# Kernel optimization log

Hardware: AMD Instinct MI355X
Metric: run time of the kernel (lower is better)

Reference implementation:

```python
import jax, jax.numpy as jnp
import numpy as np

# Model constants (from Equilibrium3BConfig + hardcoded MambaBlock args)
D_MODEL = 2560
D_INNER = 5120          # expand=2
N_STATE = 128           # d_state
HEADS = 80              # d_inner // headdim
P_HEAD = 64             # headdim
D_CONV = 4
CONV_DIM = D_INNER + 2 * N_STATE        # 5376 (x, B, C share the conv)
D_IN_PROJ = 2 * D_INNER + 2 * N_STATE + HEADS  # 10576 (z, xBC, dt)
N_EXPERTS = 16
TOP_K = 2
M_INTER = 864
MS_INTER = 1728
EPS = 1e-6


def _rms(x, w, eps=EPS):
    xf = x.astype(jnp.float32)
    xf = xf * jax.lax.rsqrt(jnp.mean(xf * xf, axis=-1, keepdims=True) + eps)
    return w * xf.astype(x.dtype)


def setup_inputs() -> dict:
    key = jax.random.key(0)
    ks = jax.random.split(key, 16)
    b, l = 1, 1024
    s = 0.02  # weight scale, keeps activations sane through the deep block
    return {
        "hidden_states": jax.random.normal(ks[0], (b, l, D_MODEL), jnp.float32),
        "w_in": jax.random.normal(ks[1], (D_MODEL, D_IN_PROJ), jnp.float32) * s,
        "conv_w": jax.random.normal(ks[2], (CONV_DIM, D_CONV), jnp.float32) * s,
        "conv_b": jnp.zeros((CONV_DIM,), jnp.float32),
        "dt_bias": jax.random.normal(ks[3], (HEADS,), jnp.float32) * s,
        "A_log": jax.random.normal(ks[4], (HEADS,), jnp.float32) * s,
        "D": jnp.ones((HEADS,), jnp.float32),
        "mamba_norm_w": jnp.ones((D_INNER,), jnp.float32),
        "w_out": jax.random.normal(ks[5], (D_INNER, D_MODEL), jnp.float32) * s,
        "ln1_w": jnp.ones((D_MODEL,), jnp.float32),
        "ln2_w": jnp.ones((D_MODEL,), jnp.float32),
        "router_w": jax.random.normal(ks[6], (D_MODEL, N_EXPERTS), jnp.float32) * s,
        "we_gate": jax.random.normal(ks[7], (N_EXPERTS, D_MODEL, M_INTER), jnp.float32) * s,
        "we_up": jax.random.normal(ks[8], (N_EXPERTS, D_MODEL, M_INTER), jnp.float32) * s,
        "we_down": jax.random.normal(ks[9], (N_EXPERTS, M_INTER, D_MODEL), jnp.float32) * s,
        "ws_gate": jax.random.normal(ks[10], (D_MODEL, MS_INTER), jnp.float32) * s,
        "ws_up": jax.random.normal(ks[11], (D_MODEL, MS_INTER), jnp.float32) * s,
        "ws_down": jax.random.normal(ks[12], (MS_INTER, D_MODEL), jnp.float32) * s,
    }


def _forward(hidden_states, w_in, conv_w, conv_b, dt_bias, A_log, D, mamba_norm_w,
             w_out, ln1_w, ln2_w, router_w, we_gate, we_up, we_down,
             ws_gate, ws_up, ws_down):
    b, l, d = hidden_states.shape

    # ---- Mamba2 (selective scan) sub-block ----
    residual = hidden_states
    x = _rms(hidden_states, ln1_w)
    zxbcdt = x @ w_in  # [b, l, 10576]
    z, xBC, dt = jnp.split(zxbcdt, [D_INNER, D_INNER + CONV_DIM], axis=-1)

    # depthwise causal conv over (x, B, C) channels, then SiLU
    xBC_t = xBC.transpose(0, 2, 1)  # [b, c, l]
    conv = jax.lax.conv_general_dilated(
        xBC_t, conv_w[:, None, :], (1,), [(D_CONV - 1, 0)],
        feature_group_count=CONV_DIM, dimension_numbers=("NCH", "OIH", "NCH"))
    xBC = jax.nn.silu((conv + conv_b[None, :, None]).transpose(0, 2, 1))
    xs, Bc, Cc = jnp.split(xBC, [D_INNER, D_INNER + N_STATE], axis=-1)

    dt = jax.nn.softplus(dt + dt_bias)          # [b, l, h]
    A = -jnp.exp(A_log)                          # [h]
    xh = xs.reshape(b, l, HEADS, P_HEAD)

    # time-major for scan
    dt_l = dt.transpose(1, 0, 2)                 # [l, b, h]
    xh_l = xh.transpose(1, 0, 2, 3)              # [l, b, h, p]
    B_l = Bc.transpose(1, 0, 2)                  # [l, b, n]
    C_l = Cc.transpose(1, 0, 2)                  # [l, b, n]

    def step(h, inp):
        dt_t, x_t, B_t, C_t = inp
        dA = jnp.exp(dt_t * A)                   # [b, h]
        h = h * dA[..., None, None] + (dt_t[..., None] * x_t)[..., None] * B_t[:, None, None, :]
        y = jnp.einsum("bhpn,bn->bhp", h, C_t)
        return h, y

    h0 = jnp.zeros((b, HEADS, P_HEAD, N_STATE), hidden_states.dtype)
    _, y_l = jax.lax.scan(step, h0, (dt_l, xh_l, B_l, C_l))
    y_l = y_l + D[None, None, :, None] * xh_l    # skip term
    y = y_l.transpose(1, 0, 2, 3).reshape(b, l, D_INNER)
    y = _rms(y * jax.nn.silu(z), mamba_norm_w)   # gated RMSNorm
    hidden = residual + y @ w_out

    # ---- DeepSeekMoE sub-block ----
    residual2 = hidden
    xm = _rms(hidden, ln2_w).reshape(b * l, d)
    logits = xm @ router_w
    probs = jax.nn.softmax(logits.astype(jnp.float32), axis=-1)
    topv, topi = jax.lax.top_k(probs, TOP_K)
    topv = topv / jnp.sum(topv, axis=-1, keepdims=True)  # renormalize top-k
    wdense = jnp.sum(jax.nn.one_hot(topi, N_EXPERTS, dtype=xm.dtype)
                     * topv[..., None].astype(xm.dtype), axis=1)  # [T, E]

    # routed experts (SwiGLU), dense-masked faithful math
    hexp = (jax.nn.silu(jnp.einsum("td,edm->tem", xm, we_gate))
            * jnp.einsum("td,edm->tem", xm, we_up))
    y_routed = jnp.einsum("tem,emd,te->td", hexp, we_down, wdense)

    # shared experts (single fused SwiGLU MLP)
    y_shared = (jax.nn.silu(xm @ ws_gate) * (xm @ ws_up)) @ ws_down

    moe = (y_routed + y_shared).reshape(b, l, d)
    return residual2 + moe


def reference(hidden_states, w_in, conv_w, conv_b, dt_bias, A_log, D, mamba_norm_w,
              w_out, ln1_w, ln2_w, router_w, we_gate, we_up, we_down,
              ws_gate, ws_up, ws_down):
    return _forward(hidden_states, w_in, conv_w, conv_b, dt_bias, A_log, D,
                    mamba_norm_w, w_out, ln1_w, ln2_w, router_w,
                    we_gate, we_up, we_down, ws_gate, ws_up, ws_down)
```

## Files before the change

### kernel.cpp

```cpp
#include <hip/hip_runtime.h>

typedef __attribute__((ext_vector_type(4))) float f32x4;
typedef __attribute__((ext_vector_type(8))) __bf16 bf16x8;
typedef __attribute__((ext_vector_type(4))) __bf16 bf16x4;
typedef __attribute__((ext_vector_type(8))) _Float16 f16x8;
typedef __attribute__((ext_vector_type(4))) _Float16 f16x4;

#define D_MODEL 2560
#define D_INNER 5120
#define N_STATE 128
#define HEADS 80
#define P_HEAD 64
#define CONV_DIM 5376
#define D_INPROJ 10576
#define SEQ 1024
#define NCHUNK 16
#define QCHUNK 64
#define NEXP 16
#define M_INTER 864
#define MS_INTER 1728
#define NSLOT 2048
#define NSLOTP 2176

__device__ __forceinline__ float siluf(float x) { return x / (1.f + __expf(-x)); }

__device__ __forceinline__ int swz_p(int k4, int P) {
  return (k4 & ~31) | ((((k4 >> 3) & 3) ^ P) << 3) | (k4 & 7);
}
__device__ __forceinline__ int swz64(int k4, int row) {
  return (k4 & ~63) | (((((k4 >> 3) & 7) ^ (row & 7)) << 3)) | (k4 & 7);
}

__device__ __forceinline__ void gl16(const __bf16* g, __bf16* l) {
  __builtin_amdgcn_global_load_lds((const __attribute__((address_space(1))) unsigned int*)g,
                                   (__attribute__((address_space(3))) unsigned int*)l, 16, 0, 0);
}

__device__ __forceinline__ float block_sum256(float v, float* red) {
#pragma unroll
  for (int m = 32; m > 0; m >>= 1) v += __shfl_xor(v, m, 64);
  int w = threadIdx.x >> 6;
  if ((threadIdx.x & 63) == 0) red[w] = v;
  __syncthreads();
  return red[0] + red[1] + red[2] + red[3];
}

template <bool FP16>
__global__ __launch_bounds__(256) void k_rmsnorm_p(const float* __restrict__ in,
                                                   const float* __restrict__ w,
                                                   float* __restrict__ f32out,
                                                   __bf16* __restrict__ ph,
                                                   __bf16* __restrict__ pdh,
                                                   __bf16* __restrict__ pdl, int D) {
  __shared__ float red[4];
  int t = blockIdx.x, tid = threadIdx.x;
  const float* x = in + (size_t)t * D;
  int nd4 = D >> 2;
  float ss = 0.f;
  for (int i = tid; i < nd4; i += 256) {
    float4 v = ((const float4*)x)[i];
    ss += v.x * v.x + v.y * v.y + v.z * v.z + v.w * v.w;
  }
  float tot = block_sum256(ss, red);
  float r = rsqrtf(tot / (float)D + 1e-6f);
  int P = (t >> 1) & 3;
  for (int i = tid; i < nd4; i += 256) {
    float4 v = ((const float4*)x)[i];
    float4 wv = ((const float4*)w)[i];
    float4 o;
    o.x = wv.x * v.x * r; o.y = wv.y * v.y * r; o.z = wv.z * v.z * r; o.w = wv.w * v.w * r;
// ... 25 lines not shown
                                                __bf16* __restrict__ Th, __bf16* __restrict__ Tl) {
  __shared__ float T[64][65];
  const int n0 = blockIdx.x * 64, k0 = blockIdx.y * 64, tid = threadIdx.x;
#pragma unroll
  for (int i = 0; i < 16; i++) {
    int idx = tid + i * 256;
    int k = idx >> 6, n = idx & 63;
    float v = 0.f;
    if (n0 + n < N) v = W[(size_t)(k0 + k) * ld + n0 + n];
    T[k][n] = v;
  }
  __syncthreads();
#pragma unroll
  for (int i = 0; i < 4; i++) {
    int idx = tid + i * 256;
    int n = idx >> 4, p4 = (idx & 15) * 4;
    int nn = n0 + n;
    if constexpr (SPLIT) {
      int P = (nn >> 1) & 3;
      bf16x4 hv, lv;
#pragma unroll
      for (int e = 0; e < 4; e++) {
        int p = p4 + e;
        int kk = (p & ~31) | ((((p >> 3) & 3) ^ P) << 3) | (p & 7);
        float v = T[kk][n];
        __bf16 h = (__bf16)v;
        hv[e] = h;
        lv[e] = (__bf16)(v - (float)h);
      }
      *(bf16x4*)&Th[(size_t)nn * K + k0 + p4] = hv;
      *(bf16x4*)&Tl[(size_t)nn * K + k0 + p4] = lv;
    } else if constexpr (FP16) {
      f16x4 hv;
#pragma unroll
      for (int e = 0; e < 4; e++) {
        int p = p4 + e;
        int kk = swz64(p, nn);
        hv[e] = (_Float16)T[kk][n];
      }
      *(f16x4*)&Th[(size_t)nn * K + k0 + p4] = hv;
    } else {
      bf16x4 hv;
#pragma unroll
      for (int e = 0; e < 4; e++) {
        int p = p4 + e;
        int kk = swz64(p, nn);
        hv[e] = (__bf16)T[kk][n];
      }
      *(bf16x4*)&Th[(size_t)nn * K + k0 + p4] = hv;
    }
  }
}

template <bool SPLIT, bool FP16, int BK>
__global__ __launch_bounds__(256) void k_gemm2(const __bf16* __restrict__ Ah,
                                               const __bf16* __restrict__ Al,
                                               const __bf16* __restrict__ Bh,
                                               const __bf16* __restrict__ Bl,
                                               float* __restrict__ C,
                                               int M, int N, int K, int ks, int nst) {
  constexpr int PLE = 128 * BK;
  constexpr int NPL = SPLIT ? 4 : 2;
  constexpr int CALLS = PLE / 2048;
  constexpr int CPR = BK / 8;
  constexpr int RPC = 256 / CPR;
  constexpr int KSUB = BK / 32;
  __shared__ __bf16 lds[NPL * PLE];
  __bf16* const AsH = lds;
  __bf16* const BsH = lds + (SPLIT ? 2 : 1) * PLE;
  __bf16* const AsL = SPLIT ? (lds + PLE) : nullptr;
  __bf16* const BsL = SPLIT ? (lds + 3 * PLE) : nullptr;

  const int tid = threadIdx.x;
  const int T = gridDim.x * gridDim.y * gridDim.z;
  const int linear = blockIdx.x + gridDim.x * (blockIdx.y + gridDim.y * blockIdx.z);
  const int s_idx = (linear & 7) * (T >> 3) + (linear >> 3);
  const int bm = s_idx & 7;
  const int g = s_idx >> 3;
  const int bn = g % gridDim.y;
  const int z = g / gridDim.y;

  const int m0 = bm * 128, n0 = bn * 128;
  const int s0 = (int)(((long long)z * nst) / ks);
  const int s1 = (int)(((long long)(z + 1) * nst) / ks);
  float* __restrict__ Cp = C + (size_t)z * M * N;

  const int lane = tid & 63, wid = tid >> 6;
  const int wr = wid >> 1, wc = wid & 1;
  const int l16 = lane & 15, kl = lane >> 4;

  const int srow = tid / CPR;
  const int schunk = (tid % CPR) * 8;
  size_t aB[CALLS], bB[CALLS];
#pragma unroll
  for (int i = 0; i < CALLS; i++) {
    aB[i] = (size_t)(m0 + srow + RPC * i) * K + schunk;
    bB[i] = (size_t)(n0 + srow + RPC * i) * K + schunk;
  }

  int aoff[4][KSUB], boff[4][KSUB];
#pragma unroll
  for (int mi = 0; mi < 4; mi++) {
    int ra = wr * 64 + mi * 16 + l16;
    int rb = wc * 64 + mi * 16 + l16;
#pragma unroll
    for (int kk = 0; kk < KSUB; kk++) {
      if constexpr (BK == 32) {
        aoff[mi][kk] = ra * 64 + ((kl ^ ((ra >> 1) & 3)) << 4);
        boff[mi][kk] = rb * 64 + ((kl ^ ((rb >> 1) & 3)) << 4);
      } else {
        aoff[mi][kk] = ra * (2 * BK) + (((kk * 4 + kl) ^ (ra & 7)) << 4);
        boff[mi][kk] = rb * (2 * BK) + (((kk * 4 + kl) ^ (rb & 7)) << 4);
      }
    }
  }

  f32x4 acc[4][4];
#pragma unroll
  for (int mi = 0; mi < 4; mi++)
#pragma unroll
    for (int ni = 0; ni < 4; ni++) acc[mi][ni] = f32x4{0.f, 0.f, 0.f, 0.f};

  for (int s = s0; s < s1; ++s) {
    const int kof = s * BK;
    __syncthreads();
#pragma unroll
    for (int i = 0; i < CALLS; i++) {
      gl16(Ah + aB[i] + kof, AsH + (tid + i * 256) * 8);
      gl16(Bh + bB[i] + kof, BsH + (tid + i * 256) * 8);
      if constexpr (SPLIT) {
        gl16(Al + aB[i] + kof, AsL + (tid + i * 256) * 8);
        gl16(Bl + bB[i] + kof, BsL + (tid + i * 256) * 8);
      }
    }
    __syncthreads();
#pragma unroll
    for (int kk = 0; kk < KSUB; kk++) {
      if constexpr (!SPLIT && FP16) {
        f16x8 ah[4], bh[4];
#pragma unroll
        for (int mi = 0; mi < 4; mi++) ah[mi] = *(const f16x8*)((const char*)AsH + aoff[mi][kk]);
#pragma unroll
        for (int ni = 0; ni < 4; ni++) bh[ni] = *(const f16x8*)((const char*)BsH + boff[ni][kk]);
#pragma unroll
        for (int mi = 0; mi < 4; mi++)
#pragma unroll
          for (int ni = 0; ni < 4; ni++)
            acc[mi][ni] = __builtin_amdgcn_mfma_f32_16x16x32_f16(ah[mi], bh[ni], acc[mi][ni], 0, 0, 0);
      } else {
        bf16x8 ah[4], bh[4];
#pragma unroll
        for (int mi = 0; mi < 4; mi++) ah[mi] = *(const bf16x8*)((const char*)AsH + aoff[mi][kk]);
#pragma unroll
        for (int ni = 0; ni < 4; ni++) bh[ni] = *(const bf16x8*)((const char*)BsH + boff[ni][kk]);
#pragma unroll
        for (int mi = 0; mi < 4; mi++)
#pragma unroll
          for (int ni = 0; ni < 4; ni++)
            acc[mi][ni] = __builtin_amdgcn_mfma_f32_16x16x32_bf16(ah[mi], bh[ni], acc[mi][ni], 0, 0, 0);
        if constexpr (SPLIT) {
          bf16x8 al[4], bl[4];
#pragma unroll
          for (int mi = 0; mi < 4; mi++) al[mi] = *(const bf16x8*)((const char*)AsL + aoff[mi][kk]);
#pragma unroll
          for (int ni = 0; ni < 4; ni++) bl[ni] = *(const bf16x8*)((const char*)BsL + boff[ni][kk]);
#pragma unroll
          for (int mi = 0; mi < 4; mi++)
#pragma unroll
            for (int ni = 0; ni < 4; ni++) {
              acc[mi][ni] = __builtin_amdgcn_mfma_f32_16x16x32_bf16(ah[mi], bl[ni], acc[mi][ni], 0, 0, 0);
              acc[mi][ni] = __builtin_amdgcn_mfma_f32_16x16x32_bf16(al[mi], bh[ni], acc[mi][ni], 0, 0, 0);
            }
        }
      }
    }
  }
#pragma unroll
  for (int mi = 0; mi < 4; mi++)
#pragma unroll
    for (int ni = 0; ni < 4; ni++)
#pragma unroll
      for (int r = 0; r < 4; r++) {
        int row = m0 + wr * 64 + mi * 16 + kl * 4 + r;
        int col = n0 + wc * 64 + ni * 16 + l16;
        if (col < N) Cp[(size_t)row * N + col] = acc[mi][ni][r];
      }
}

template <bool RES>
__global__ void k_reduce(const float* __restrict__ Pp, int np, int n4,
                         const float* __restrict__ res, float* __restrict__ out) {
  int i = blockIdx.x * 256 + threadIdx.x;
  int stride = gridDim.x * 256;
  for (; i < n4; i += stride) {
    float4 a = ((const float4*)Pp)[i];
    for (int z = 1; z < np; z++) {
      float4 b = ((const float4*)Pp)[(size_t)z * n4 + i];
      a.x += b.x; a.y += b.y; a.z += b.z; a.w += b.w;
    }
    if constexpr (RES) {
      float4 r0 = ((const float4*)res)[i];
      a.x += r0.x; a.y += r0.y; a.z += r0.z; a.w += r0.w;
    }
    ((float4*)out)[i] = a;
  }
}

__global__ void k_dtfin(const float* __restrict__ dtP, const float* __restrict__ dt_bias,
                        const float* __restrict__ A_log, float* __restrict__ dtp,
                        float* __restrict__ dtA) {
  int t = blockIdx.x, h = threadIdx.x;
  if (h < HEADS) {
    float v = dt_bias[h];
#pragma unroll
    for (int z = 0; z < 8; z++) v += dtP[((size_t)z * SEQ + t) * 80 + h];
    float sp = fmaxf(v, 0.f) + log1pf(expf(-fabsf(v)));
    dtp[t * HEADS + h] = sp;
    dtA[t * HEADS + h] = sp * (-expf(A_log[h]));
  }
}

__global__ __launch_bounds__(256) void k_gatherA(const float* __restrict__ xm,
                                                 const int* __restrict__ perm,
                                                 __bf16* __restrict__ Aslots) {
  int s = blockIdx.x, tid = threadIdx.x;
  int t = perm[s];
  int P = (s >> 1) & 3;
  const float* src = xm + (size_t)t * D_MODEL;
  __bf16* dst = Aslots + (size_t)s * D_MODEL;
// ... 113 lines not shown
          int rl = bm * 128 + wr * 64 + mi * 16 + kl * 4 + r;
          int col = n0 + wc * 64 + ni * 16 + l16;
          if (rl < cnt && col < N) Cpl[(size_t)(base + rl) * N + col] = acc[mi][ni][r];
        }
  }
}

__global__ __launch_bounds__(256) void k_silumulE(const float* __restrict__ gP,
                                                  const float* __restrict__ uP,
                                                  const float* __restrict__ slotw,
                                                  __bf16* __restrict__ outp) {
  int s = blockIdx.x, tid = threadIdx.x;
  float w = slotw[s];
  int P = (s >> 1) & 3;
  const size_t PL = (size_t)NSLOTP * M_INTER;
  for (int i = tid; i < M_INTER / 4; i += 256) {
    f32x4 g = f32x4{0.f, 0.f, 0.f, 0.f}, u = f32x4{0.f, 0.f, 0.f, 0.f};
#pragma unroll
    for (int z = 0; z < 4; z++) {
      g += *(const f32x4*)&gP[z * PL + (size_t)s * M_INTER + i * 4];
      u += *(const f32x4*)&uP[z * PL + (size_t)s * M_INTER + i * 4];
    }
    int p = swz_p(i * 4, P);
    bf16x4 h;
    h[0] = (__bf16)(siluf(g[0]) * u[0] * w);
    h[1] = (__bf16)(siluf(g[1]) * u[1] * w);
    h[2] = (__bf16)(siluf(g[2]) * u[2] * w);
    h[3] = (__bf16)(siluf(g[3]) * u[3] * w);
    *(bf16x4*)&outp[(size_t)s * M_INTER + p] = h;
  }
}

__global__ __launch_bounds__(256) void k_silumul_sh2(const float* __restrict__ P4,
                                                     __bf16* __restrict__ outp) {
  int t = blockIdx.x, tid = threadIdx.x;
  const size_t PL = (size_t)SEQ * 3456;
  for (int i = tid; i < MS_INTER / 4; i += 256) {
    f32x4 g = f32x4{0.f, 0.f, 0.f, 0.f}, u = f32x4{0.f, 0.f, 0.f, 0.f};
#pragma unroll
    for (int z = 0; z < 4; z++) {
      g += *(const f32x4*)&P4[z * PL + (size_t)t * 3456 + i * 4];
      u += *(const f32x4*)&P4[z * PL + (size_t)t * 3456 + 1728 + i * 4];
    }
    int p = swz64(i * 4, t);
    bf16x4 h;
    h[0] = (__bf16)(siluf(g[0]) * u[0]);
    h[1] = (__bf16)(siluf(g[1]) * u[1]);
    h[2] = (__bf16)(siluf(g[2]) * u[2]);
    h[3] = (__bf16)(siluf(g[3]) * u[3]);
    *(bf16x4*)&outp[(size_t)t * MS_INTER + p] = h;
  }
}

__global__ void k_conv(const float* __restrict__ zx0, const float* __restrict__ zx1,
                       const float* __restrict__ cw, const float* __restrict__ cb,
                       float* __restrict__ xBC) {
  int cidx = blockIdx.x * 256 + threadIdx.x;
  int t = blockIdx.y;
  if (cidx < CONV_DIM) {
    float acc = cb[cidx];
#pragma unroll
    for (int j = 0; j < 4; j++) {
      int tt = t - 3 + j;
      if (tt >= 0) {
        size_t idx = (size_t)tt * D_INPROJ + D_INNER + cidx;
        acc += (zx0[idx] + zx1[idx]) * cw[cidx * 4 + j];
      }
    }
    xBC[(size_t)t * CONV_DIM + cidx] = siluf(acc);
  }
}

__global__ __launch_bounds__(256) void k_scan_intra(
    const float* __restrict__ xBC, const float* __restrict__ dtp,
    const float* __restrict__ dtA, float* __restrict__ y, float* __restrict__ S,
    float* __restrict__ cumA, float* __restrict__ Atot) {
  __shared__ float Bs[64][132];
  __shared__ float Cs[64][132];
  __shared__ float Xs[64][68];
  __shared__ float Gs[64][65];
  __shared__ float da_s[64], a_s[64], dt_sh[64], w_sh[64];
  int c = blockIdx.x, h = blockIdx.y, tid = threadIdx.x;
  int t0 = c * QCHUNK;
#pragma unroll
  for (int i = 0; i < 8; i++) {
    int id = tid + 256 * i;
    int r = id >> 5, c4 = (id & 31) * 4;
    *(float4*)&Bs[r][c4] = *(const float4*)&xBC[(size_t)(t0 + r) * CONV_DIM + D_INNER + c4];
    *(float4*)&Cs[r][c4] = *(const float4*)&xBC[(size_t)(t0 + r) * CONV_DIM + D_INNER + N_STATE + c4];
  }
#pragma unroll
  for (int i = 0; i < 4; i++) {
    int id = tid + 256 * i;
    int r = id >> 4, p4 = (id & 15) * 4;
    *(float4*)&Xs[r][p4] = *(const float4*)&xBC[(size_t)(t0 + r) * CONV_DIM + h * P_HEAD + p4];
  }
  if (tid < 64) {
    da_s[tid] = dtA[(size_t)(t0 + tid) * HEADS + h];
    dt_sh[tid] = dtp[(size_t)(t0 + tid) * HEADS + h];
  }
  __syncthreads();
  if (tid < 64) {
    float a = 0.f;
    for (int i = 0; i <= tid; i++) a += da_s[i];
    a_s[tid] = a;
    cumA[((size_t)c * HEADS + h) * 64 + tid] = a;
  }
  __syncthreads();
  if (tid < 64) {
    w_sh[tid] = __expf(a_s[63] - a_s[tid]) * dt_sh[tid];
    if (tid == 0) Atot[c * HEADS + h] = a_s[63];
  }
  __syncthreads();
  {
    int tq = tid >> 4, sq = tid & 15;
    float gacc[4][4];
#pragma unroll
    for (int j = 0; j < 4; j++)
#pragma unroll
      for (int jj = 0; jj < 4; jj++) gacc[j][jj] = 0.f;
    for (int n4 = 0; n4 < 128; n4 += 4) {
      float4 cv[4], bv[4];
#pragma unroll
      for (int j = 0; j < 4; j++) cv[j] = *(const float4*)&Cs[tq * 4 + j][n4];
#pragma unroll
      for (int j = 0; j < 4; j++) bv[j] = *(const float4*)&Bs[sq * 4 + j][n4];
#pragma unroll
      for (int j = 0; j < 4; j++)
#pragma unroll
        for (int jj = 0; jj < 4; jj++)
          gacc[j][jj] += cv[j].x * bv[jj].x + cv[j].y * bv[jj].y + cv[j].z * bv[jj].z + cv[j].w * bv[jj].w;
    }
#pragma unroll
    for (int j = 0; j < 4; j++)
#pragma unroll
      for (int jj = 0; jj < 4; jj++) {
        int t = tq * 4 + j, s = sq * 4 + jj;
        float arg = fminf(a_s[t] - a_s[s], 0.f);
        Gs[t][s] = (s <= t) ? gacc[j][jj] * __expf(arg) * dt_sh[s] : 0.f;
      }
  }
  __syncthreads();
  {
    int tq = tid >> 4, pq = tid & 15;
    float4 acc[4];
#pragma unroll
    for (int j = 0; j < 4; j++) acc[j] = float4{0.f, 0.f, 0.f, 0.f};
    for (int s = 0; s < 64; s++) {
      float4 xv = *(const float4*)&Xs[s][pq * 4];
#pragma unroll
      for (int j = 0; j < 4; j++) {
        float g = Gs[tq * 4 + j][s];
        acc[j].x += g * xv.x; acc[j].y += g * xv.y; acc[j].z += g * xv.z; acc[j].w += g * xv.w;
      }
    }
#pragma unroll
    for (int j = 0; j < 4; j++) {
      int t = tq * 4 + j;
      *(float4*)&y[(size_t)(t0 + t) * D_INNER + h * P_HEAD + pq * 4] = acc[j];
    }
  }
  {
    int p2 = tid >> 5, n4 = (tid & 31) * 4;
    float4 acc[8];
#pragma unroll
    for (int j = 0; j < 8; j++) acc[j] = float4{0.f, 0.f, 0.f, 0.f};
    for (int s = 0; s < 64; s++) {
      float4 bv = *(const float4*)&Bs[s][n4];
#pragma unroll
      for (int j = 0; j < 8; j++) {
        float xw = Xs[s][p2 * 8 + j] * w_sh[s];
        acc[j].x += xw * bv.x; acc[j].y += xw * bv.y; acc[j].z += xw * bv.z; acc[j].w += xw * bv.w;
      }
    }
    size_t bb = ((size_t)(c * HEADS + h) * 64) * 128;
#pragma unroll
    for (int j = 0; j < 8; j++)
      *(float4*)&S[bb + (size_t)(p2 * 8 + j) * 128 + n4] = acc[j];
  }
}

__global__ void k_scan_state(float* __restrict__ S, const float* __restrict__ Atot) {
  int gid = blockIdx.x * 256 + threadIdx.x;
  int h = gid >> 13;
  int rem = gid & 8191;
  float run = 0.f;
#pragma unroll
  for (int c = 0; c < NCHUNK; c++) {
    size_t idx = ((size_t)(c * HEADS + h) << 13) + rem;
    float s = S[idx];
    S[idx] = run;
    run = run * __expf(Atot[c * HEADS + h]) + s;
  }
}

__global__ __launch_bounds__(256) void k_scan_inter(
    const float* __restrict__ xBC, const float* __restrict__ Hin,
    const float* __restrict__ cumA, const float* __restrict__ Dv,
    float* __restrict__ y) {
  __shared__ float Hs[64][132];
  __shared__ float Cs[64][132];
  __shared__ float a_l[64];
  int c = blockIdx.x, h = blockIdx.y, tid = threadIdx.x;
  int t0 = c * QCHUNK;
#pragma unroll
  for (int i = 0; i < 8; i++) {
    int id = tid + 256 * i;
    int r = id >> 5, n4 = (id & 31) * 4;
    *(float4*)&Hs[r][n4] = *(const float4*)&Hin[(((size_t)(c * HEADS + h) * 64 + r) << 7) + n4];
    *(float4*)&Cs[r][n4] = *(const float4*)&xBC[(size_t)(t0 + r) * CONV_DIM + D_INNER + N_STATE + n4];
  }
  if (tid < 64) a_l[tid] = cumA[((size_t)c * HEADS + h) * 64 + tid];
  __syncthreads();
  float Dh = Dv[h];
  int tq = tid >> 4, pq = tid & 15;
  float4 acc[4];
#pragma unroll
  for (int j = 0; j < 4; j++) acc[j] = float4{0.f, 0.f, 0.f, 0.f};
  for (int n4 = 0; n4 < 128; n4 += 4) {
    float4 hv[4], cv[4];
#pragma unroll
    for (int jj = 0; jj < 4; jj++) hv[jj] = *(const float4*)&Hs[pq * 4 + jj][n4];
#pragma unroll
    for (int j = 0; j < 4; j++) cv[j] = *(const float4*)&Cs[tq * 4 + j][n4];
#pragma unroll
    for (int j = 0; j < 4; j++) {
      acc[j].x += cv[j].x * hv[0].x + cv[j].y * hv[0].y + cv[j].z * hv[0].z + cv[j].w * hv[0].w;
      acc[j].y += cv[j].x * hv[1].x + cv[j].y * hv[1].y + cv[j].z * hv[1].z + cv[j].w * hv[1].w;
      acc[j].z += cv[j].x * hv[2].x + cv[j].y * hv[2].y + cv[j].z * hv[2].z + cv[j].w * hv[2].w;
      acc[j].w += cv[j].x * hv[3].x + cv[j].y * hv[3].y + cv[j].z * hv[3].z + cv[j].w * hv[3].w;
    }
  }
#pragma unroll
  for (int j = 0; j < 4; j++) {
    int t = tq * 4 + j;
    float e = __expf(a_l[t]);
    float4 xv = *(const float4*)&xBC[(size_t)(t0 + t) * CONV_DIM + h * P_HEAD + pq * 4];
    size_t yoff = (size_t)(t0 + t) * D_INNER + h * P_HEAD + pq * 4;
    float4 yv = *(float4*)&y[yoff];
    yv.x += e * acc[j].x + Dh * xv.x;
    yv.y += e * acc[j].y + Dh * xv.y;
    yv.z += e * acc[j].z + Dh * xv.z;
    yv.w += e * acc[j].w + Dh * xv.w;
    *(float4*)&y[yoff] = yv;
  }
}

__global__ __launch_bounds__(256) void k_gatednorm_p(const float* __restrict__ y,
                                                     const float* __restrict__ zx0,
                                                     const float* __restrict__ zx1,
                                                     const float* __restrict__ w,
                                                     __bf16* __restrict__ ph) {
  __shared__ float vbuf[D_INNER];
  __shared__ float red[4];
  int t = blockIdx.x, tid = threadIdx.x;
  float ss = 0.f;
  for (int i = tid; i < D_INNER / 4; i += 256) {
    float4 yv = *(const float4*)&y[(size_t)t * D_INNER + i * 4];
    f32x4 z0 = *(const f32x4*)&zx0[(size_t)t * D_INPROJ + i * 4];
    f32x4 z1 = *(const f32x4*)&zx1[(size_t)t * D_INPROJ + i * 4];
    f32x4 zs = z0 + z1;
    float4 v;
    v.x = yv.x * siluf(zs[0]); v.y = yv.y * siluf(zs[1]);
    v.z = yv.z * siluf(zs[2]); v.w = yv.w * siluf(zs[3]);
    *(float4*)&vbuf[i * 4] = v;
    ss += v.x * v.x + v.y * v.y + v.z * v.z + v.w * v.w;
  }
  float tot = block_sum256(ss, red);
  float r = rsqrtf(tot / (float)D_INNER + 1e-6f);
  for (int i = tid; i < D_INNER / 4; i += 256) {
    float4 v = *(const float4*)&vbuf[i * 4];
    float4 wv = *(const float4*)&w[i * 4];
    float4 o;
    o.x = wv.x * v.x * r; o.y = wv.y * v.y * r; o.z = wv.z * v.z * r; o.w = wv.w * v.w * r;
    int p = swz64(i * 4, t);
    f16x4 hv;
    hv[0] = (_Float16)o.x; hv[1] = (_Float16)o.y; hv[2] = (_Float16)o.z; hv[3] = (_Float16)o.w;
    *(f16x4*)&ph[(size_t)t * D_INNER + p] = hv;
  }
}

__global__ void k_zero(int* counts, int* cursor) {
  int i = threadIdx.x;
  if (i < NEXP) { counts[i] = 0; cursor[i] = 0; }
}

__global__ __launch_bounds__(256) void k_router(const float* __restrict__ xm,
                                                const float* __restrict__ Wr,
                                                int* __restrict__ top_i,
                                                float* __restrict__ top_v,
                                                int* __restrict__ counts) {
  __shared__ float part[16][17];
  __shared__ float lg[16];
  int t = blockIdx.x, tid = threadIdx.x;
  int e = tid & 15, seg = tid >> 4;
  const float* xr = xm + (size_t)t * D_MODEL;
  float s = 0.f;
  for (int i = 0; i < 160; i++) {
    int k = seg * 160 + i;
    s += xr[k] * Wr[(size_t)k * NEXP + e];
  }
  part[seg][e] = s;
  __syncthreads();
  if (tid < 16) {
    float l = 0.f;
    for (int g = 0; g < 16; g++) l += part[g][tid];
    lg[tid] = l;
  }
  __syncthreads();
  if (tid == 0) {
    float mx = lg[0];
    for (int i = 1; i < 16; i++) mx = fmaxf(mx, lg[i]);
    float pe[16];
    for (int i = 0; i < 16; i++) pe[i] = expf(lg[i] - mx);
    int i0 = 0; float v0 = pe[0];
    for (int i = 1; i < 16; i++) if (pe[i] > v0) { v0 = pe[i]; i0 = i; }
    int i1 = -1; float v1 = -1.f;
// ... 32 lines not shown
                         const float* __restrict__ dsP, const int* __restrict__ slotOf,
                         float* __restrict__ out) {
  int t = blockIdx.y;
  int d4 = (blockIdx.x * 256 + threadIdx.x) * 4;
  if (d4 < D_MODEL) {
    int s0 = slotOf[t * 2], s1 = slotOf[t * 2 + 1];
    f32x4 a = *(const f32x4*)&hidden[(size_t)t * D_MODEL + d4];
    f32x4 b = *(const f32x4*)&sh[(size_t)t * D_MODEL + d4];
    f32x4 acc = a + b;
    const size_t PL = (size_t)NSLOTP * D_MODEL;
#pragma unroll
    for (int z = 0; z < 3; z++) {
      acc += *(const f32x4*)&dsP[z * PL + (size_t)s0 * D_MODEL + d4];
      acc += *(const f32x4*)&dsP[z * PL + (size_t)s1 * D_MODEL + d4];
    }
    *(f32x4*)&out[(size_t)t * D_MODEL + d4] = acc;
  }
}

extern "C" void kernel_launch(void* const* d_in, const int* in_sizes, int n_in,
                              void* d_out, int out_size, void* d_ws, size_t ws_size,
                              hipStream_t stream) {
  const float* hs = (const float*)d_in[0];
  const float* w_in = (const float*)d_in[1];
  const float* conv_w = (const float*)d_in[2];
  const float* conv_b = (const float*)d_in[3];
  const float* dt_bias = (const float*)d_in[4];
  const float* A_log = (const float*)d_in[5];
  const float* Dv = (const float*)d_in[6];
  const float* mnw = (const float*)d_in[7];
  const float* w_out = (const float*)d_in[8];
  const float* ln1 = (const float*)d_in[9];
  const float* ln2 = (const float*)d_in[10];
  const float* router_w = (const float*)d_in[11];
  const float* we_gate = (const float*)d_in[12];
  const float* we_up = (const float*)d_in[13];
  const float* we_down = (const float*)d_in[14];
  const float* ws_gate = (const float*)d_in[15];
  const float* ws_up = (const float*)d_in[16];
  const float* ws_down = (const float*)d_in[17];

  char* base = (char*)d_ws;
  size_t off = 0;
  auto A = [&](size_t bytes) -> void* {
    void* p = base + off;
    off += (bytes + 255) & ~(size_t)255;
    return p;
  };
  float* xbc = (float*)A((size_t)SEQ * CONV_DIM * 4);
  float* xmf = (float*)A((size_t)SEQ * D_MODEL * 4);
  float* dtp = (float*)A((size_t)SEQ * HEADS * 4);
  float* dtA = (float*)A((size_t)SEQ * HEADS * 4);
  float* yf = (float*)A((size_t)SEQ * D_INNER * 4);
  float* cumA = (float*)A((size_t)NCHUNK * HEADS * 64 * 4);
  float* Atot = (float*)A((size_t)NCHUNK * HEADS * 4);
  float* Sbuf = (float*)A((size_t)NCHUNK * HEADS * 64 * 128 * 4);
  float* hidden = (float*)A((size_t)SEQ * D_MODEL * 4);
  float* shout = (float*)A((size_t)SEQ * D_MODEL * 4);
  float* top_v = (float*)A(8192);
  float* slotw = (float*)A(8192);
  int* top_i = (int*)A(8192);
  int* counts = (int*)A(64);
  int* offs = (int*)A(64);
  int* cursor = (int*)A(64);
  int* perm = (int*)A(8192);
  int* slotOf = (int*)A(8192);
  __bf16* xp_h = (__bf16*)A((size_t)SEQ * D_MODEL * 2);
  __bf16* ybp_h = (__bf16*)A((size_t)SEQ * D_INNER * 2);
  __bf16* gbuf_bh = (__bf16*)A((size_t)SEQ * MS_INTER * 2);
  char* REG = (char*)A((size_t)163000000);

  __bf16* winT_h = (__bf16*)REG;
  float* zxP = (float*)(REG + 60000000);
  const size_t ZXPL = (size_t)SEQ * D_INPROJ;
  __bf16* xdt_h = (__bf16*)(REG + 147000000);
  __bf16* xdt_l = (__bf16*)(REG + 152500000);
  __bf16* wdt_h = (__bf16*)(REG + 158000000);
  __bf16* wdt_l = (__bf16*)(REG + 158700000);
  float* dtP = (float*)(REG + 159400000);
  __bf16* woutT_h = (__bf16*)REG;
  float* partials = (float*)(REG + 60000000);
  __bf16* guT = (__bf16*)REG;
  __bf16* downT = (__bf16*)(REG + 18350080);
  float* partials4 = (float*)(REG + 30000000);
  __bf16* Aslots = (__bf16*)REG;
  __bf16* gsl = (__bf16*)(REG + 12000000);
  float* gateP = (float*)(REG + 16000000);
  float* upP = (float*)(REG + 47000000);
  float* dslotsP = (float*)(REG + 78000000);

  k_rmsnorm_p<true><<<SEQ, 256, 0, stream>>>(hs, ln1, nullptr, xp_h, xdt_h, xdt_l, D_MODEL);
  k_transW<false, true><<<dim3(166, 40), 256, 0, stream>>>(w_in, D_INPROJ, D_MODEL, D_INPROJ,
                                                           winT_h, nullptr);
  k_transW<true, false><<<dim3(2, 40), 256, 0, stream>>>(w_in + 10496, D_INPROJ, D_MODEL, 80,
                                                         wdt_h, wdt_l);
  k_gemm2<false, true, 64><<<dim3(8, 83, 2), 256, 0, stream>>>(xp_h, nullptr, winT_h, nullptr, zxP,
                                                               SEQ, D_INPROJ, D_MODEL, 2, 40);
  k_gemm2<true, false, 32><<<dim3(8, 1, 8), 256, 0, stream>>>(xdt_h, xdt_l, wdt_h, wdt_l, dtP,
                                                              SEQ, 80, D_MODEL, 8, 80);
  k_dtfin<<<SEQ, 128, 0, stream>>>(dtP, dt_bias, A_log, dtp, dtA);
  k_conv<<<dim3(21, SEQ), 256, 0, stream>>>(zxP, zxP + ZXPL, conv_w, conv_b, xbc);
  k_scan_intra<<<dim3(NCHUNK, HEADS), 256, 0, stream>>>(xbc, dtp, dtA, yf, Sbuf, cumA, Atot);
  k_scan_state<<<2560, 256, 0, stream>>>(Sbuf, Atot);
  k_scan_inter<<<dim3(NCHUNK, HEADS), 256, 0, stream>>>(xbc, Sbuf, cumA, Dv, yf);
  k_gatednorm_p<<<SEQ, 256, 0, stream>>>(yf, zxP, zxP + ZXPL, mnw, ybp_h);
  k_transW<false, true><<<dim3(40, 80), 256, 0, stream>>>(w_out, D_MODEL, D_INNER, D_MODEL,
                                                          woutT_h, nullptr);
  k_gemm2<false, true, 64><<<dim3(8, 20, 4), 256, 0, stream>>>(ybp_h, nullptr, woutT_h, nullptr,
                                                               partials, SEQ, D_MODEL, D_INNER, 4, 80);
  k_reduce<true><<<2048, 256, 0, stream>>>(partials, 4, SEQ * D_MODEL / 4, hs, hidden);

  k_rmsnorm_p<false><<<SEQ, 256, 0, stream>>>(hidden, ln2, xmf, xp_h, nullptr, nullptr, D_MODEL);
  k_zero<<<1, 64, 0, stream>>>(counts, cursor);
  k_router<<<SEQ, 256, 0, stream>>>(xmf, router_w, top_i, top_v, counts);
  k_offsets<<<1, 32, 0, stream>>>(counts, offs, cursor);
  k_scatter<<<4, 256, 0, stream>>>(top_i, top_v, cursor, perm, slotOf, slotw);

  k_transW<false, false><<<dim3(27, 40), 256, 0, stream>>>(ws_gate, MS_INTER, D_MODEL, MS_INTER,
                                                           guT, nullptr);
  k_transW<false, false><<<dim3(27, 40), 256, 0, stream>>>(ws_up, MS_INTER, D_MODEL, MS_INTER,
                                                           guT + (size_t)MS_INTER * D_MODEL, nullptr);
  k_gemm2<false, false, 64><<<dim3(8, 27, 4), 256, 0, stream>>>(xp_h, nullptr, guT, nullptr,
                                                                partials4, SEQ, 3456, D_MODEL, 4, 40);
  k_silumul_sh2<<<SEQ, 256, 0, stream>>>(partials4, gbuf_bh);
  k_transW<false, false><<<dim3(40, 27), 256, 0, stream>>>(ws_down, D_MODEL, MS_INTER, D_MODEL,
                                                           downT, nullptr);
  k_gemm2<false, false, 64><<<dim3(8, 20, 4), 256, 0, stream>>>(gbuf_bh, nullptr, downT, nullptr,
                                                                partials4, SEQ, D_MODEL, MS_INTER, 4, 27);
  k_reduce<false><<<2048, 256, 0, stream>>>(partials4, 4, SEQ * D_MODEL / 4, nullptr, shout);

  k_gatherA<<<NSLOT, 256, 0, stream>>>(xmf, perm, Aslots);
  k_gemmE2<4><<<dim3(7, 4, NEXP), 256, 0, stream>>>(Aslots, we_gate, gateP, offs, counts,
                                                    M_INTER, D_MODEL, (long long)D_MODEL * M_INTER);
  k_gemmE2<4><<<dim3(7, 4, NEXP), 256, 0, stream>>>(Aslots, we_up, upP, offs, counts,
                                                    M_INTER, D_MODEL, (long long)D_MODEL * M_INTER);
  k_silumulE<<<NSLOT, 256, 0, stream>>>(gateP, upP, slotw, gsl);
  k_gemmE2<3><<<dim3(20, 3, NEXP), 256, 0, stream>>>(gsl, we_down, dslotsP, offs, counts,
                                                     D_MODEL, M_INTER, (long long)M_INTER * D_MODEL);

  k_final2<<<dim3(3, SEQ), 256, 0, stream>>>(hidden, shout, dslotsP, slotOf, (float*)d_out);
}
```

Measured before the change: 850.6 us.

## Double-buffer GEMM LDS staging, drop in-proj split-K, halve scan chunk size

```diff
diff --git a/kernel.cpp b/kernel.cpp
--- a/kernel.cpp
+++ b/kernel.cpp
@@ -14,8 +14,8 @@
 #define CONV_DIM 5376
 #define D_INPROJ 10576
 #define SEQ 1024
-#define NCHUNK 16
-#define QCHUNK 64
+#define NCHUNK 32
+#define QCHUNK 32
 #define NEXP 16
 #define M_INTER 864
 #define MS_INTER 1728
@@ -147,7 +147,7 @@
   }
 }
 
-template <bool SPLIT, bool FP16, int BK>
+template <bool SPLIT, bool FP16, int BK, bool PIPE>
 __global__ __launch_bounds__(256) void k_gemm2(const __bf16* __restrict__ Ah,
                                                const __bf16* __restrict__ Al,
                                                const __bf16* __restrict__ Bh,
@@ -156,15 +156,12 @@
                                                int M, int N, int K, int ks, int nst) {
   constexpr int PLE = 128 * BK;
   constexpr int NPL = SPLIT ? 4 : 2;
+  constexpr int NBUF = PIPE ? 2 : 1;
   constexpr int CALLS = PLE / 2048;
   constexpr int CPR = BK / 8;
   constexpr int RPC = 256 / CPR;
   constexpr int KSUB = BK / 32;
-  __shared__ __bf16 lds[NPL * PLE];
-  __bf16* const AsH = lds;
-  __bf16* const BsH = lds + (SPLIT ? 2 : 1) * PLE;
-  __bf16* const AsL = SPLIT ? (lds + PLE) : nullptr;
-  __bf16* const BsL = SPLIT ? (lds + 3 * PLE) : nullptr;
+  __shared__ __bf16 lds[NBUF * NPL * PLE];
 
   const int tid = threadIdx.x;
   const int T = gridDim.x * gridDim.y * gridDim.z;
@@ -216,27 +213,30 @@
 #pragma unroll
     for (int ni = 0; ni < 4; ni++) acc[mi][ni] = f32x4{0.f, 0.f, 0.f, 0.f};
 
-  for (int s = s0; s < s1; ++s) {
-    const int kof = s * BK;
-    __syncthreads();
+  auto STAGE = [&](int b, int kof) {
+    __bf16* L = lds + (size_t)b * NPL * PLE;
 #pragma unroll
     for (int i = 0; i < CALLS; i++) {
-      gl16(Ah + aB[i] + kof, AsH + (tid + i * 256) * 8);
-      gl16(Bh + bB[i] + kof, BsH + (tid + i * 256) * 8);
+      gl16(Ah + aB[i] + kof, L + (tid + i * 256) * 8);
+      gl16(Bh + bB[i] + kof, L + (SPLIT ? 2 : 1) * PLE + (tid + i * 256) * 8);
       if constexpr (SPLIT) {
-        gl16(Al + aB[i] + kof, AsL + (tid + i * 256) * 8);
-        gl16(Bl + bB[i] + kof, BsL + (tid + i * 256) * 8);
-      }
-    }
-    __syncthreads();
+        gl16(Al + aB[i] + kof, L + PLE + (tid + i * 256) * 8);
+        gl16(Bl + bB[i] + kof, L + 3 * PLE + (tid + i * 256) * 8);
+      }
+    }
+  };
+
+  auto COMPUTE = [&](const __bf16* L) {
+    const char* AsH = (const char*)L;
+    const char* BsH = (const char*)(L + (SPLIT ? 2 : 1) * PLE);
 #pragma unroll
     for (int kk = 0; kk < KSUB; kk++) {
       if constexpr (!SPLIT && FP16) {
         f16x8 ah[4], bh[4];
 #pragma unroll
-        for (int mi = 0; mi < 4; mi++) ah[mi] = *(const f16x8*)((const char*)AsH + aoff[mi][kk]);
-#pragma unroll
-        for (int ni = 0; ni < 4; ni++) bh[ni] = *(const f16x8*)((const char*)BsH + boff[ni][kk]);
+        for (int mi = 0; mi < 4; mi++) ah[mi] = *(const f16x8*)(AsH + aoff[mi][kk]);
+#pragma unroll
+        for (int ni = 0; ni < 4; ni++) bh[ni] = *(const f16x8*)(BsH + boff[ni][kk]);
 #pragma unroll
         for (int mi = 0; mi < 4; mi++)
 #pragma unroll
@@ -245,20 +245,22 @@
       } else {
         bf16x8 ah[4], bh[4];
 #pragma unroll
-        for (int mi = 0; mi < 4; mi++) ah[mi] = *(const bf16x8*)((const char*)AsH + aoff[mi][kk]);
-#pragma unroll
-        for (int ni = 0; ni < 4; ni++) bh[ni] = *(const bf16x8*)((const char*)BsH + boff[ni][kk]);
+        for (int mi = 0; mi < 4; mi++) ah[mi] = *(const bf16x8*)(AsH + aoff[mi][kk]);
+#pragma unroll
+        for (int ni = 0; ni < 4; ni++) bh[ni] = *(const bf16x8*)(BsH + boff[ni][kk]);
 #pragma unroll
         for (int mi = 0; mi < 4; mi++)
 #pragma unroll
           for (int ni = 0; ni < 4; ni++)
             acc[mi][ni] = __builtin_amdgcn_mfma_f32_16x16x32_bf16(ah[mi], bh[ni], acc[mi][ni], 0, 0, 0);
         if constexpr (SPLIT) {
+          const char* AsL = (const char*)(L + PLE);
+          const char* BsL = (const char*)(L + 3 * PLE);
           bf16x8 al[4], bl[4];
 #pragma unroll
-          for (int mi = 0; mi < 4; mi++) al[mi] = *(const bf16x8*)((const char*)AsL + aoff[mi][kk]);
-#pragma unroll
-          for (int ni = 0; ni < 4; ni++) bl[ni] = *(const bf16x8*)((const char*)BsL + boff[ni][kk]);
+          for (int mi = 0; mi < 4; mi++) al[mi] = *(const bf16x8*)(AsL + aoff[mi][kk]);
+#pragma unroll
+          for (int ni = 0; ni < 4; ni++) bl[ni] = *(const bf16x8*)(BsL + boff[ni][kk]);
 #pragma unroll
           for (int mi = 0; mi < 4; mi++)
 #pragma unroll
@@ -269,7 +271,27 @@
         }
       }
     }
-  }
+  };
+
+  if constexpr (PIPE) {
+    STAGE(0, s0 * BK);
+    __syncthreads();
+    int cur = 0;
+    for (int s = s0; s < s1; ++s) {
+      if (s + 1 < s1) STAGE(cur ^ 1, (s + 1) * BK);
+      COMPUTE(lds + (size_t)cur * NPL * PLE);
+      __syncthreads();
+      cur ^= 1;
+    }
+  } else {
+    for (int s = s0; s < s1; ++s) {
+      __syncthreads();
+      STAGE(0, s * BK);
+      __syncthreads();
+      COMPUTE(lds);
+    }
+  }
+
 #pragma unroll
   for (int mi = 0; mi < 4; mi++)
 #pragma unroll
@@ -489,9 +511,8 @@
   }
 }
 
-__global__ void k_conv(const float* __restrict__ zx0, const float* __restrict__ zx1,
-                       const float* __restrict__ cw, const float* __restrict__ cb,
-                       float* __restrict__ xBC) {
+__global__ void k_conv(const float* __restrict__ zx, const float* __restrict__ cw,
+                       const float* __restrict__ cb, float* __restrict__ xBC) {
   int cidx = blockIdx.x * 256 + threadIdx.x;
   int t = blockIdx.y;
   if (cidx < CONV_DIM) {
@@ -499,10 +520,7 @@
 #pragma unroll
     for (int j = 0; j < 4; j++) {
       int tt = t - 3 + j;
-      if (tt >= 0) {
-        size_t idx = (size_t)tt * D_INPROJ + D_INNER + cidx;
-        acc += (zx0[idx] + zx1[idx]) * cw[cidx * 4 + j];
-      }
+      if (tt >= 0) acc += zx[(size_t)tt * D_INPROJ + D_INNER + cidx] * cw[cidx * 4 + j];
     }
     xBC[(size_t)t * CONV_DIM + cidx] = siluf(acc);
   }
@@ -512,67 +530,67 @@
     const float* __restrict__ xBC, const float* __restrict__ dtp,
     const float* __restrict__ dtA, float* __restrict__ y, float* __restrict__ S,
     float* __restrict__ cumA, float* __restrict__ Atot) {
-  __shared__ float Bs[64][132];
-  __shared__ float Cs[64][132];
-  __shared__ float Xs[64][68];
-  __shared__ float Gs[64][65];
-  __shared__ float da_s[64], a_s[64], dt_sh[64], w_sh[64];
+  __shared__ float Bs[32][128];
+  __shared__ float Cs[32][128];
+  __shared__ float Xs[32][68];
+  __shared__ float Gs[32][33];
+  __shared__ float da_s[32], a_s[32], dt_sh[32], w_sh[32];
   int c = blockIdx.x, h = blockIdx.y, tid = threadIdx.x;
   int t0 = c * QCHUNK;
 #pragma unroll
-  for (int i = 0; i < 8; i++) {
+  for (int i = 0; i < 4; i++) {
     int id = tid + 256 * i;
-    int r = id >> 5, c4 = (id & 31) * 4;
-    *(float4*)&Bs[r][c4] = *(const float4*)&xBC[(size_t)(t0 + r) * CONV_DIM + D_INNER + c4];
-    *(float4*)&Cs[r][c4] = *(const float4*)&xBC[(size_t)(t0 + r) * CONV_DIM + D_INNER + N_STATE + c4];
-  }
-#pragma unroll
-  for (int i = 0; i < 4; i++) {
+    int r = id >> 5, cc = id & 31;
+    int sc = (cc ^ (r & 31)) * 4;
+    *(float4*)&Bs[r][sc] = *(const float4*)&xBC[(size_t)(t0 + r) * CONV_DIM + D_INNER + cc * 4];
+    *(float4*)&Cs[r][sc] = *(const float4*)&xBC[(size_t)(t0 + r) * CONV_DIM + D_INNER + N_STATE + cc * 4];
+  }
+#pragma unroll
+  for (int i = 0; i < 2; i++) {
     int id = tid + 256 * i;
     int r = id >> 4, p4 = (id & 15) * 4;
     *(float4*)&Xs[r][p4] = *(const float4*)&xBC[(size_t)(t0 + r) * CONV_DIM + h * P_HEAD + p4];
   }
-  if (tid < 64) {
+  if (tid < 32) {
     da_s[tid] = dtA[(size_t)(t0 + tid) * HEADS + h];
     dt_sh[tid] = dtp[(size_t)(t0 + tid) * HEADS + h];
   }
   __syncthreads();
-  if (tid < 64) {
+  if (tid < 32) {
     float a = 0.f;
     for (int i = 0; i <= tid; i++) a += da_s[i];
     a_s[tid] = a;
-    cumA[((size_t)c * HEADS + h) * 64 + tid] = a;
+    cumA[((size_t)c * HEADS + h) * QCHUNK + tid] = a;
   }
   __syncthreads();
-  if (tid < 64) {
-    w_sh[tid] = __expf(a_s[63] - a_s[tid]) * dt_sh[tid];
-    if (tid == 0) Atot[c * HEADS + h] = a_s[63];
+  if (tid < 32) {
+    w_sh[tid] = __expf(a_s[31] - a_s[tid]) * dt_sh[tid];
+    if (tid == 0) Atot[c * HEADS + h] = a_s[31];
   }
   __syncthreads();
   {
     int tq = tid >> 4, sq = tid & 15;
-    float gacc[4][4];
-#pragma unroll
-    for (int j = 0; j < 4; j++)
-#pragma unroll
-      for (int jj = 0; jj < 4; jj++) gacc[j][jj] = 0.f;
-    for (int n4 = 0; n4 < 128; n4 += 4) {
-      float4 cv[4], bv[4];
-#pragma unroll
-      for (int j = 0; j < 4; j++) cv[j] = *(const float4*)&Cs[tq * 4 + j][n4];
-#pragma unroll
-      for (int j = 0; j < 4; j++) bv[j] = *(const float4*)&Bs[sq * 4 + j][n4];
-#pragma unroll
-      for (int j = 0; j < 4; j++)
-#pragma unroll
-        for (int jj = 0; jj < 4; jj++)
+    float gacc[2][2] = {{0.f, 0.f}, {0.f, 0.f}};
+    for (int nc = 0; nc < 32; nc++) {
+      float4 cv[2], bv[2];
+#pragma unroll
+      for (int j = 0; j < 2; j++) {
+        int rt = tq * 2 + j;
+        cv[j] = *(const float4*)&Cs[rt][(nc ^ (rt & 31)) * 4];
+        int rs = sq * 2 + j;
+        bv[j] = *(const float4*)&Bs[rs][(nc ^ (rs & 31)) * 4];
+      }
+#pragma unroll
+      for (int j = 0; j < 2; j++)
+#pragma unroll
+        for (int jj = 0; jj < 2; jj++)
           gacc[j][jj] += cv[j].x * bv[jj].x + cv[j].y * bv[jj].y + cv[j].z * bv[jj].z + cv[j].w * bv[jj].w;
     }
 #pragma unroll
-    for (int j = 0; j < 4; j++)
-#pragma unroll
-      for (int jj = 0; jj < 4; jj++) {
-        int t = tq * 4 + j, s = sq * 4 + jj;
+    for (int j = 0; j < 2; j++)
+#pragma unroll
+      for (int jj = 0; jj < 2; jj++) {
+        int t = tq * 2 + j, s = sq * 2 + jj;
         float arg = fminf(a_s[t] - a_s[s], 0.f);
         Gs[t][s] = (s <= t) ? gacc[j][jj] * __expf(arg) * dt_sh[s] : 0.f;
       }
@@ -580,40 +598,40 @@
   __syncthreads();
   {
     int tq = tid >> 4, pq = tid & 15;
-    float4 acc[4];
-#pragma unroll
-    for (int j = 0; j < 4; j++) acc[j] = float4{0.f, 0.f, 0.f, 0.f};
-    for (int s = 0; s < 64; s++) {
+    float4 acc[2];
+    acc[0] = float4{0.f, 0.f, 0.f, 0.f};
+    acc[1] = float4{0.f, 0.f, 0.f, 0.f};
+    for (int s = 0; s < 32; s++) {
       float4 xv = *(const float4*)&Xs[s][pq * 4];
 #pragma unroll
-      for (int j = 0; j < 4; j++) {
-        float g = Gs[tq * 4 + j][s];
-        acc[j].x += g * xv.x; acc[j].y += g * xv.y; acc[j].z += g * xv.z; acc[j].w += g * xv.w;
-      }
-    }
-#pragma unroll
-    for (int j = 0; j < 4; j++) {
-      int t = tq * 4 + j;
+      for (int j = 0; j < 2; j++) {
+        float g0 = Gs[tq * 2 + j][s];
+        acc[j].x += g0 * xv.x; acc[j].y += g0 * xv.y; acc[j].z += g0 * xv.z; acc[j].w += g0 * xv.w;
+      }
+    }
+#pragma unroll
+    for (int j = 0; j < 2; j++) {
+      int t = tq * 2 + j;
       *(float4*)&y[(size_t)(t0 + t) * D_INNER + h * P_HEAD + pq * 4] = acc[j];
     }
   }
   {
-    int p2 = tid >> 5, n4 = (tid & 31) * 4;
+    int p2 = tid >> 5, ncc = tid & 31;
     float4 acc[8];
 #pragma unroll
     for (int j = 0; j < 8; j++) acc[j] = float4{0.f, 0.f, 0.f, 0.f};
-    for (int s = 0; s < 64; s++) {
-      float4 bv = *(const float4*)&Bs[s][n4];
+    for (int s = 0; s < 32; s++) {
+      float4 bvv = *(const float4*)&Bs[s][(ncc ^ (s & 31)) * 4];
 #pragma unroll
       for (int j = 0; j < 8; j++) {
         float xw = Xs[s][p2 * 8 + j] * w_sh[s];
-        acc[j].x += xw * bv.x; acc[j].y += xw * bv.y; acc[j].z += xw * bv.z; acc[j].w += xw * bv.w;
+        acc[j].x += xw * bvv.x; acc[j].y += xw * bvv.y; acc[j].z += xw * bvv.z; acc[j].w += xw * bvv.w;
       }
     }
     size_t bb = ((size_t)(c * HEADS + h) * 64) * 128;
 #pragma unroll
     for (int j = 0; j < 8; j++)
-      *(float4*)&S[bb + (size_t)(p2 * 8 + j) * 128 + n4] = acc[j];
+      *(float4*)&S[bb + (size_t)(p2 * 8 + j) * 128 + ncc * 4] = acc[j];
   }
 }
 
@@ -635,33 +653,46 @@
     const float* __restrict__ xBC, const float* __restrict__ Hin,
     const float* __restrict__ cumA, const float* __restrict__ Dv,
     float* __restrict__ y) {
-  __shared__ float Hs[64][132];
-  __shared__ float Cs[64][132];
-  __shared__ float a_l[64];
+  __shared__ float Hs[64][128];
+  __shared__ float Cs[32][128];
+  __shared__ float a_l[32];
   int c = blockIdx.x, h = blockIdx.y, tid = threadIdx.x;
   int t0 = c * QCHUNK;
 #pragma unroll
   for (int i = 0; i < 8; i++) {
     int id = tid + 256 * i;
-    int r = id >> 5, n4 = (id & 31) * 4;
-    *(float4*)&Hs[r][n4] = *(const float4*)&Hin[(((size_t)(c * HEADS + h) * 64 + r) << 7) + n4];
-    *(float4*)&Cs[r][n4] = *(const float4*)&xBC[(size_t)(t0 + r) * CONV_DIM + D_INNER + N_STATE + n4];
-  }
-  if (tid < 64) a_l[tid] = cumA[((size_t)c * HEADS + h) * 64 + tid];
+    int r = id >> 5, cc = id & 31;
+    *(float4*)&Hs[r][(cc ^ (r & 31)) * 4] =
+        *(const float4*)&Hin[(((size_t)(c * HEADS + h) * 64 + r) << 7) + cc * 4];
+  }
+#pragma unroll
+  for (int i = 0; i < 4; i++) {
+    int id = tid + 256 * i;
+    int r = id >> 5, cc = id & 31;
+    *(float4*)&Cs[r][(cc ^ (r & 31)) * 4] =
+        *(const float4*)&xBC[(size_t)(t0 + r) * CONV_DIM + D_INNER + N_STATE + cc * 4];
+  }
+  if (tid < 32) a_l[tid] = cumA[((size_t)c * HEADS + h) * QCHUNK + tid];
   __syncthreads();
   float Dh = Dv[h];
   int tq = tid >> 4, pq = tid & 15;
-  float4 acc[4];
-#pragma unroll
-  for (int j = 0; j < 4; j++) acc[j] = float4{0.f, 0.f, 0.f, 0.f};
-  for (int n4 = 0; n4 < 128; n4 += 4) {
-    float4 hv[4], cv[4];
-#pragma unroll
-    for (int jj = 0; jj < 4; jj++) hv[jj] = *(const float4*)&Hs[pq * 4 + jj][n4];
-#pragma unroll
-    for (int j = 0; j < 4; j++) cv[j] = *(const float4*)&Cs[tq * 4 + j][n4];
-#pragma unroll
-    for (int j = 0; j < 4; j++) {
+  float4 acc[2];
+  acc[0] = float4{0.f, 0.f, 0.f, 0.f};
+  acc[1] = float4{0.f, 0.f, 0.f, 0.f};
+  for (int nc = 0; nc < 32; nc++) {
+    float4 cv[2], hv[4];
+#pragma unroll
+    for (int j = 0; j < 2; j++) {
+      int rt = tq * 2 + j;
+      cv[j] = *(const float4*)&Cs[rt][(nc ^ (rt & 31)) * 4];
+    }
+#pragma unroll
+    for (int jj = 0; jj < 4; jj++) {
+      int rp = pq * 4 + jj;
+      hv[jj] = *(const float4*)&Hs[rp][(nc ^ (rp & 31)) * 4];
+    }
+#pragma unroll
+    for (int j = 0; j < 2; j++) {
       acc[j].x += cv[j].x * hv[0].x + cv[j].y * hv[0].y + cv[j].z * hv[0].z + cv[j].w * hv[0].w;
       acc[j].y += cv[j].x * hv[1].x + cv[j].y * hv[1].y + cv[j].z * hv[1].z + cv[j].w * hv[1].w;
       acc[j].z += cv[j].x * hv[2].x + cv[j].y * hv[2].y + cv[j].z * hv[2].z + cv[j].w * hv[2].w;
@@ -669,8 +700,8 @@
     }
   }
 #pragma unroll
-  for (int j = 0; j < 4; j++) {
-    int t = tq * 4 + j;
+  for (int j = 0; j < 2; j++) {
+    int t = tq * 2 + j;
     float e = __expf(a_l[t]);
     float4 xv = *(const float4*)&xBC[(size_t)(t0 + t) * CONV_DIM + h * P_HEAD + pq * 4];
     size_t yoff = (size_t)(t0 + t) * D_INNER + h * P_HEAD + pq * 4;
@@ -684,8 +715,7 @@
 }
 
 __global__ __launch_bounds__(256) void k_gatednorm_p(const float* __restrict__ y,
-                                                     const float* __restrict__ zx0,
-                                                     const float* __restrict__ zx1,
+                                                     const float* __restrict__ zx,
                                                      const float* __restrict__ w,
                                                      __bf16* __restrict__ ph) {
   __shared__ float vbuf[D_INNER];
@@ -694,12 +724,10 @@
   float ss = 0.f;
   for (int i = tid; i < D_INNER / 4; i += 256) {
     float4 yv = *(const float4*)&y[(size_t)t * D_INNER + i * 4];
-    f32x4 z0 = *(const f32x4*)&zx0[(size_t)t * D_INPROJ + i * 4];
-    f32x4 z1 = *(const f32x4*)&zx1[(size_t)t * D_INPROJ + i * 4];
-    f32x4 zs = z0 + z1;
+    float4 zv = *(const float4*)&zx[(size_t)t * D_INPROJ + i * 4];
     float4 v;
-    v.x = yv.x * siluf(zs[0]); v.y = yv.y * siluf(zs[1]);
-    v.z = yv.z * siluf(zs[2]); v.w = yv.w * siluf(zs[3]);
+    v.x = yv.x * siluf(zv.x); v.y = yv.y * siluf(zv.y);
+    v.z = yv.z * siluf(zv.z); v.w = yv.w * siluf(zv.w);
     *(float4*)&vbuf[i * 4] = v;
     ss += v.x * v.x + v.y * v.y + v.z * v.z + v.w * v.w;
   }
@@ -838,7 +866,7 @@
   float* dtp = (float*)A((size_t)SEQ * HEADS * 4);
   float* dtA = (float*)A((size_t)SEQ * HEADS * 4);
   float* yf = (float*)A((size_t)SEQ * D_INNER * 4);
-  float* cumA = (float*)A((size_t)NCHUNK * HEADS * 64 * 4);
+  float* cumA = (float*)A((size_t)NCHUNK * HEADS * QCHUNK * 4);
   float* Atot = (float*)A((size_t)NCHUNK * HEADS * 4);
   float* Sbuf = (float*)A((size_t)NCHUNK * HEADS * 64 * 128 * 4);
   float* hidden = (float*)A((size_t)SEQ * D_MODEL * 4);
@@ -857,15 +885,14 @@
   char* REG = (char*)A((size_t)163000000);
 
   __bf16* winT_h = (__bf16*)REG;
-  float* zxP = (float*)(REG + 60000000);
-  const size_t ZXPL = (size_t)SEQ * D_INPROJ;
+  float* zx = (float*)(REG + 60000000);
+  float* partials = (float*)(REG + 104000000);
   __bf16* xdt_h = (__bf16*)(REG + 147000000);
   __bf16* xdt_l = (__bf16*)(REG + 152500000);
   __bf16* wdt_h = (__bf16*)(REG + 158000000);
   __bf16* wdt_l = (__bf16*)(REG + 158700000);
   float* dtP = (float*)(REG + 159400000);
   __bf16* woutT_h = (__bf16*)REG;
-  float* partials = (float*)(REG + 60000000);
   __bf16* guT = (__bf16*)REG;
   __bf16* downT = (__bf16*)(REG + 18350080);
   float* partials4 = (float*)(REG + 30000000);
@@ -880,20 +907,20 @@
                                                            winT_h, nullptr);
   k_transW<true, false><<<dim3(2, 40), 256, 0, stream>>>(w_in + 10496, D_INPROJ, D_MODEL, 80,
                                                          wdt_h, wdt_l);
-  k_gemm2<false, true, 64><<<dim3(8, 83, 2), 256, 0, stream>>>(xp_h, nullptr, winT_h, nullptr, zxP,
-                                                               SEQ, D_INPROJ, D_MODEL, 2, 40);
-  k_gemm2<true, false, 32><<<dim3(8, 1, 8), 256, 0, stream>>>(xdt_h, xdt_l, wdt_h, wdt_l, dtP,
-                                                              SEQ, 80, D_MODEL, 8, 80);
+  k_gemm2<false, true, 64, true><<<dim3(8, 83, 1), 256, 0, stream>>>(
+      xp_h, nullptr, winT_h, nullptr, zx, SEQ, D_INPROJ, D_MODEL, 1, 40);
+  k_gemm2<true, false, 32, false><<<dim3(8, 1, 8), 256, 0, stream>>>(
+      xdt_h, xdt_l, wdt_h, wdt_l, dtP, SEQ, 80, D_MODEL, 8, 80);
   k_dtfin<<<SEQ, 128, 0, stream>>>(dtP, dt_bias, A_log, dtp, dtA);
-  k_conv<<<dim3(21, SEQ), 256, 0, stream>>>(zxP, zxP + ZXPL, conv_w, conv_b, xbc);
+  k_conv<<<dim3(21, SEQ), 256, 0, stream>>>(zx, conv_w, conv_b, xbc);
   k_scan_intra<<<dim3(NCHUNK, HEADS), 256, 0, stream>>>(xbc, dtp, dtA, yf, Sbuf, cumA, Atot);
   k_scan_state<<<2560, 256, 0, stream>>>(Sbuf, Atot);
   k_scan_inter<<<dim3(NCHUNK, HEADS), 256, 0, stream>>>(xbc, Sbuf, cumA, Dv, yf);
-  k_gatednorm_p<<<SEQ, 256, 0, stream>>>(yf, zxP, zxP + ZXPL, mnw, ybp_h);
+  k_gatednorm_p<<<SEQ, 256, 0, stream>>>(yf, zx, mnw, ybp_h);
   k_transW<false, true><<<dim3(40, 80), 256, 0, stream>>>(w_out, D_MODEL, D_INNER, D_MODEL,
                                                           woutT_h, nullptr);
-  k_gemm2<false, true, 64><<<dim3(8, 20, 4), 256, 0, stream>>>(ybp_h, nullptr, woutT_h, nullptr,
-                                                               partials, SEQ, D_MODEL, D_INNER, 4, 80);
+  k_gemm2<false, true, 64, true><<<dim3(8, 20, 4), 256, 0, stream>>>(
+      ybp_h, nullptr, woutT_h, nullptr, partials, SEQ, D_MODEL, D_INNER, 4, 80);
   k_reduce<true><<<2048, 256, 0, stream>>>(partials, 4, SEQ * D_MODEL / 4, hs, hidden);
 
   k_rmsnorm_p<false><<<SEQ, 256, 0, stream>>>(hidden, ln2, xmf, xp_h, nullptr, nullptr, D_MODEL);
@@ -906,13 +933,13 @@
                                                            guT, nullptr);
   k_transW<false, false><<<dim3(27, 40), 256, 0, stream>>>(ws_up, MS_INTER, D_MODEL, MS_INTER,
                                                            guT + (size_t)MS_INTER * D_MODEL, nullptr);
-  k_gemm2<false, false, 64><<<dim3(8, 27, 4), 256, 0, stream>>>(xp_h, nullptr, guT, nullptr,
-                                                                partials4, SEQ, 3456, D_MODEL, 4, 40);
+  k_gemm2<false, false, 64, true><<<dim3(8, 27, 4), 256, 0, stream>>>(
+      xp_h, nullptr, guT, nullptr, partials4, SEQ, 3456, D_MODEL, 4, 40);
   k_silumul_sh2<<<SEQ, 256, 0, stream>>>(partials4, gbuf_bh);
   k_transW<false, false><<<dim3(40, 27), 256, 0, stream>>>(ws_down, D_MODEL, MS_INTER, D_MODEL,
                                                            downT, nullptr);
-  k_gemm2<false, false, 64><<<dim3(8, 20, 4), 256, 0, stream>>>(gbuf_bh, nullptr, downT, nullptr,
-                                                                partials4, SEQ, D_MODEL, MS_INTER, 4, 27);
+  k_gemm2<false, false, 64, true><<<dim3(8, 20, 4), 256, 0, stream>>>(
+      gbuf_bh, nullptr, downT, nullptr, partials4, SEQ, D_MODEL, MS_INTER, 4, 27);
   k_reduce<false><<<2048, 256, 0, stream>>>(partials4, 4, SEQ * D_MODEL / 4, nullptr, shout);
 
   k_gatherA<<<NSLOT, 256, 0, stream>>>(xmf, perm, Aslots);
```

After: 877.6 us. 1.03x slower.
